# Performance work log

Measured on AMD Instinct MI355X. Metric: run time of the kernel, lower is better.

The kernel has to match this reference:

```python
import jax, jax.numpy as jnp
import numpy as np

N0, N1, N2, D, FANOUT = 900000, 43008, 2048, 64, 20


def setup_inputs() -> dict:
    key = jax.random.key(0)
    ks = jax.random.split(key, 8)
    x = jax.random.normal(ks[0], (N0, D), jnp.float32)
    edge_src0 = jax.random.randint(ks[1], (N1 * FANOUT,), 0, N0, jnp.int32)
    edge_dst0 = jax.random.randint(ks[2], (N1 * FANOUT,), 0, N1, jnp.int32)
    edge_src1 = jax.random.randint(ks[3], (N2 * FANOUT,), 0, N1, jnp.int32)
    edge_dst1 = jax.random.randint(ks[4], (N2 * FANOUT,), 0, N2, jnp.int32)
    # torch Linear(2D, D): store transposed as [2D, D] for x @ w + b
    w0 = jax.random.normal(ks[5], (2 * D, D), jnp.float32) * 0.05
    w1 = jax.random.normal(ks[6], (2 * D, D), jnp.float32) * 0.05
    b0 = jnp.zeros((D,), jnp.float32)
    b1 = jnp.zeros((D,), jnp.float32)
    return {"x": x, "w0": w0, "b0": b0, "w1": w1, "b1": b1,
            "edge_src0": edge_src0, "edge_dst0": edge_dst0,
            "edge_src1": edge_src1, "edge_dst1": edge_dst1,
            "n1": N1, "n2": N2}


def _sage_layer(h, src, dst, n_tgt, w, b, relu):
    # gather neighbor features [E, D]
    source_x = h[src]
    # scatter-mean into targets (torch_scatter reduce='mean' with zero init:
    # targets with no incoming edges stay 0)
    summ = jax.ops.segment_sum(source_x, dst, num_segments=n_tgt)
    cnt = jax.ops.segment_sum(jnp.ones((src.shape[0], 1), h.dtype), dst,
                              num_segments=n_tgt)
    aggr = summ / jnp.maximum(cnt, 1.0)
    out = jnp.concatenate([h[:n_tgt], aggr], axis=1) @ w + b
    return jax.nn.relu(out) if relu else out


def reference(x, w0, b0, w1, b1, edge_src0, edge_dst0, edge_src1, edge_dst1, n1, n2):
    # dropout is identity in eval mode
    h = _sage_layer(x, edge_src0, edge_dst0, n1, w0, b0, relu=True)
    out = _sage_layer(h, edge_src1, edge_dst1, n2, w1, b1, relu=False)
    return out
```

## Files before the change

kernel.cpp:

```cpp
#include <hip/hip_runtime.h>


#define D 64
constexpr int N1c = 43008;
constexpr int N2c = 2048;
constexpr int CAP = 64;

static __device__ __forceinline__ float readlane_f(float v, int l) {
    return __builtin_bit_cast(float, __builtin_amdgcn_readlane(__builtin_bit_cast(int, v), l));
}

__global__ void fill2_kernel(const int* __restrict__ es0, const int* __restrict__ ed0, int E0,
                             const int* __restrict__ es1, const int* __restrict__ ed1, int E1,
                             int* __restrict__ deg0, int* __restrict__ bucket0,
                             int* __restrict__ deg1, int* __restrict__ bucket1) {
    int t = blockIdx.x * blockDim.x + threadIdx.x;
    if (t < E0) {
        int d = ed0[t];
        int pos = atomicAdd(&deg0[d], 1);
        if (pos < CAP) bucket0[(size_t)d * CAP + pos] = es0[t];
    } else if (t - E0 < E1) {
        int e = t - E0;
        int d = ed1[e];
        int pos = atomicAdd(&deg1[d], 1);
        if (pos < CAP) bucket1[(size_t)d * CAP + pos] = es1[e];
    }
}

template <int BASE>
static __device__ __forceinline__ float slots32(int dg, int sidx,
                                                const float* __restrict__ feat,
                                                int lane) {
    float a0 = 0.f, a1 = 0.f, a2 = 0.f, a3 = 0.f;
#pragma unroll
    for (int j = 0; j < 32; j += 4) {
        int s0 = __builtin_amdgcn_readlane(sidx, BASE + j + 0);
        int s1 = __builtin_amdgcn_readlane(sidx, BASE + j + 1);
        int s2 = __builtin_amdgcn_readlane(sidx, BASE + j + 2);
        int s3 = __builtin_amdgcn_readlane(sidx, BASE + j + 3);
        float v0 = feat[(size_t)s0 * D + lane];
        float v1 = feat[(size_t)s1 * D + lane];
        float v2 = feat[(size_t)s2 * D + lane];
        float v3 = feat[(size_t)s3 * D + lane];
        a0 += (BASE + j + 0 < dg) ? v0 : 0.f;
        a1 += (BASE + j + 1 < dg) ? v1 : 0.f;
        a2 += (BASE + j + 2 < dg) ? v2 : 0.f;
        a3 += (BASE + j + 3 < dg) ? v3 : 0.f;
    }
    return (a0 + a1) + (a2 + a3);
}

__global__ void __launch_bounds__(256)
aggr_kernel(const float* __restrict__ feat,
            const int* __restrict__ deg, const int* __restrict__ bucket,
            float* __restrict__ aggr, int nrows) {
    int i = blockIdx.x * 4 + (threadIdx.x >> 6);
    int lane = threadIdx.x & 63;
    if (i >= nrows) return;
    int dgt = deg[i];
    int dg = dgt > CAP ? CAP : dgt;

    int sidx = (lane < dg) ? bucket[(size_t)i * CAP + lane] : 0;

    float sum = slots32<0>(dg, sidx, feat, lane);
    if (dg > 32)
        sum += slots32<32>(dg, sidx, feat, lane);

    float inv = 1.0f / fmaxf((float)dgt, 1.0f);
    aggr[(size_t)i * D + lane] = sum * inv;
}

__global__ void __launch_bounds__(256)
dense_kernel(const float* __restrict__ self_feat, const float* __restrict__ aggr,
             const float* __restrict__ w, const float* __restrict__ b,
             float* __restrict__ out, int nrows, int do_relu) {
    __shared__ float wlds[2 * D * D];
    int tid = threadIdx.x;
    {
        const float4* wsrc = (const float4*)w;
        float4* wdst = (float4*)wlds;
#pragma unroll
        for (int t = 0; t < 8; ++t)
            wdst[t * 256 + tid] = wsrc[t * 256 + tid];
    }
    __syncthreads();

    int wv = tid >> 6, lane = tid & 63;
    int i0 = (blockIdx.x * 4 + wv) * 4;
    if (i0 >= nrows) return;

    float x0 = self_feat[(size_t)(i0 + 0) * D + lane];
    float x1 = self_feat[(size_t)(i0 + 1) * D + lane];
    float x2 = self_feat[(size_t)(i0 + 2) * D + lane];
    float x3 = self_feat[(size_t)(i0 + 3) * D + lane];
    float g0 = aggr[(size_t)(i0 + 0) * D + lane];
    float g1 = aggr[(size_t)(i0 + 1) * D + lane];
    float g2 = aggr[(size_t)(i0 + 2) * D + lane];
    float g3 = aggr[(size_t)(i0 + 3) * D + lane];

    float bb = b[lane];
    float o0 = bb, o1 = bb, o2 = bb, o3 = bb;

#pragma unroll 16
    for (int k = 0; k < D; ++k) {
        float ws = wlds[k * D + lane];
        float wa = wlds[(D + k) * D + lane];
        o0 += readlane_f(x0, k) * ws + readlane_f(g0, k) * wa;
        o1 += readlane_f(x1, k) * ws + readlane_f(g1, k) * wa;
        o2 += readlane_f(x2, k) * ws + readlane_f(g2, k) * wa;
        o3 += readlane_f(x3, k) * ws + readlane_f(g3, k) * wa;
    }
    if (do_relu) {
        o0 = fmaxf(o0, 0.f); o1 = fmaxf(o1, 0.f);
        o2 = fmaxf(o2, 0.f); o3 = fmaxf(o3, 0.f);
    }
    out[(size_t)(i0 + 0) * D + lane] = o0;
    out[(size_t)(i0 + 1) * D + lane] = o1;
    out[(size_t)(i0 + 2) * D + lane] = o2;
    out[(size_t)(i0 + 3) * D + lane] = o3;
}

extern "C" void kernel_launch(void* const* d_in, const int* in_sizes, int n_in,
                              void* d_out, int out_size, void* d_ws, size_t ws_size,
                              hipStream_t stream) {
    const float* x   = (const float*)d_in[0];
    const float* w0  = (const float*)d_in[1];
    const float* b0  = (const float*)d_in[2];
    const float* w1  = (const float*)d_in[3];
    const float* b1  = (const float*)d_in[4];
    const int* es0   = (const int*)d_in[5];
    const int* ed0   = (const int*)d_in[6];
    const int* es1   = (const int*)d_in[7];
    const int* ed1   = (const int*)d_in[8];
    const int E0 = in_sizes[5];
    const int E1 = in_sizes[7];

    int* deg0    = (int*)d_ws;
    int* deg1    = deg0 + N1c;
    int* bucket0 = deg1 + N2c;
    int* bucket1 = bucket0 + (size_t)N1c * CAP;
    float* ag0   = (float*)(bucket1 + (size_t)N2c * CAP);
    float* h     = ag0 + (size_t)N1c * D;
    float* ag1   = h + (size_t)N1c * D;

    hipMemsetAsync(d_ws, 0, (size_t)(N1c + N2c) * sizeof(int), stream);

    int total = E0 + E1;
    fill2_kernel<<<(total + 255) / 256, 256, 0, stream>>>(es0, ed0, E0, es1, ed1, E1,
                                                          deg0, bucket0, deg1, bucket1);

    aggr_kernel<<<N1c / 4, 256, 0, stream>>>(x, deg0, bucket0, ag0, N1c);
    dense_kernel<<<N1c / 16, 256, 0, stream>>>(x, ag0, w0, b0, h, N1c, 1);

    aggr_kernel<<<N2c / 4, 256, 0, stream>>>(h, deg1, bucket1, ag1, N2c);
    dense_kernel<<<N2c / 16, 256, 0, stream>>>(h, ag1, w1, b1, (float*)d_out, N2c, 0);
}
```

Measured before the change: 411.7 us.

## Fuse neighbor aggregation into dense layer kernel and vectorize edge bucketing

Merges the aggregation and dense-projection kernels into one per-layer kernel, so the aggregated features stay in registers and no intermediate buffer is written to or read back from global memory. The aggregation now always issues 32 or 64 gathers without per-slot masking. Invalid slots read row 0, and the extra contribution is subtracted afterwards, which can cause small floating-point differences. The bucketing kernel now processes four edges per thread with int4 loads, which assumes E0 and E1 are multiples of four and that the arrays are suitably aligned.

```diff
diff --git a/kernel.cpp b/kernel.cpp
--- a/kernel.cpp
+++ b/kernel.cpp
@@ -15,22 +15,33 @@
                              int* __restrict__ deg0, int* __restrict__ bucket0,
                              int* __restrict__ deg1, int* __restrict__ bucket1) {
     int t = blockIdx.x * blockDim.x + threadIdx.x;
-    if (t < E0) {
-        int d = ed0[t];
-        int pos = atomicAdd(&deg0[d], 1);
-        if (pos < CAP) bucket0[(size_t)d * CAP + pos] = es0[t];
-    } else if (t - E0 < E1) {
-        int e = t - E0;
-        int d = ed1[e];
-        int pos = atomicAdd(&deg1[d], 1);
-        if (pos < CAP) bucket1[(size_t)d * CAP + pos] = es1[e];
+    int base = t * 4;
+    if (base < E0) {
+        int4 d4 = *(const int4*)(ed0 + base);
+        int4 s4 = *(const int4*)(es0 + base);
+        int p;
+        p = atomicAdd(&deg0[d4.x], 1); if (p < CAP) bucket0[(size_t)d4.x * CAP + p] = s4.x;
+        p = atomicAdd(&deg0[d4.y], 1); if (p < CAP) bucket0[(size_t)d4.y * CAP + p] = s4.y;
+        p = atomicAdd(&deg0[d4.z], 1); if (p < CAP) bucket0[(size_t)d4.z * CAP + p] = s4.z;
+        p = atomicAdd(&deg0[d4.w], 1); if (p < CAP) bucket0[(size_t)d4.w * CAP + p] = s4.w;
+    } else {
+        int b1 = base - E0;
+        if (b1 < E1) {
+            int4 d4 = *(const int4*)(ed1 + b1);
+            int4 s4 = *(const int4*)(es1 + b1);
+            int p;
+            p = atomicAdd(&deg1[d4.x], 1); if (p < CAP) bucket1[(size_t)d4.x * CAP + p] = s4.x;
+            p = atomicAdd(&deg1[d4.y], 1); if (p < CAP) bucket1[(size_t)d4.y * CAP + p] = s4.y;
+            p = atomicAdd(&deg1[d4.z], 1); if (p < CAP) bucket1[(size_t)d4.z * CAP + p] = s4.z;
+            p = atomicAdd(&deg1[d4.w], 1); if (p < CAP) bucket1[(size_t)d4.w * CAP + p] = s4.w;
+        }
     }
 }
 
 template <int BASE>
-static __device__ __forceinline__ float slots32(int dg, int sidx,
-                                                const float* __restrict__ feat,
-                                                int lane) {
+static __device__ __forceinline__ float slots32u(int sidx,
+                                                 const float* __restrict__ feat,
+                                                 int lane) {
     float a0 = 0.f, a1 = 0.f, a2 = 0.f, a3 = 0.f;
 #pragma unroll
     for (int j = 0; j < 32; j += 4) {
@@ -38,42 +49,19 @@
         int s1 = __builtin_amdgcn_readlane(sidx, BASE + j + 1);
         int s2 = __builtin_amdgcn_readlane(sidx, BASE + j + 2);
         int s3 = __builtin_amdgcn_readlane(sidx, BASE + j + 3);
-        float v0 = feat[(size_t)s0 * D + lane];
-        float v1 = feat[(size_t)s1 * D + lane];
-        float v2 = feat[(size_t)s2 * D + lane];
-        float v3 = feat[(size_t)s3 * D + lane];
-        a0 += (BASE + j + 0 < dg) ? v0 : 0.f;
-        a1 += (BASE + j + 1 < dg) ? v1 : 0.f;
-        a2 += (BASE + j + 2 < dg) ? v2 : 0.f;
-        a3 += (BASE + j + 3 < dg) ? v3 : 0.f;
+        a0 += feat[(size_t)s0 * D + lane];
+        a1 += feat[(size_t)s1 * D + lane];
+        a2 += feat[(size_t)s2 * D + lane];
+        a3 += feat[(size_t)s3 * D + lane];
     }
     return (a0 + a1) + (a2 + a3);
 }
 
 __global__ void __launch_bounds__(256)
-aggr_kernel(const float* __restrict__ feat,
-            const int* __restrict__ deg, const int* __restrict__ bucket,
-            float* __restrict__ aggr, int nrows) {
-    int i = blockIdx.x * 4 + (threadIdx.x >> 6);
-    int lane = threadIdx.x & 63;
-    if (i >= nrows) return;
-    int dgt = deg[i];
-    int dg = dgt > CAP ? CAP : dgt;
-
-    int sidx = (lane < dg) ? bucket[(size_t)i * CAP + lane] : 0;
-
-    float sum = slots32<0>(dg, sidx, feat, lane);
-    if (dg > 32)
-        sum += slots32<32>(dg, sidx, feat, lane);
-
-    float inv = 1.0f / fmaxf((float)dgt, 1.0f);
-    aggr[(size_t)i * D + lane] = sum * inv;
-}
-
-__global__ void __launch_bounds__(256)
-dense_kernel(const float* __restrict__ self_feat, const float* __restrict__ aggr,
-             const float* __restrict__ w, const float* __restrict__ b,
-             float* __restrict__ out, int nrows, int do_relu) {
+fused_layer_kernel(const float* __restrict__ feat,
+                   const int* __restrict__ deg, const int* __restrict__ bucket,
+                   const float* __restrict__ w, const float* __restrict__ b,
+                   float* __restrict__ out, int do_relu) {
     __shared__ float wlds[2 * D * D];
     int tid = threadIdx.x;
     {
@@ -87,28 +75,34 @@
 
     int wv = tid >> 6, lane = tid & 63;
     int i0 = (blockIdx.x * 4 + wv) * 4;
-    if (i0 >= nrows) return;
 
-    float x0 = self_feat[(size_t)(i0 + 0) * D + lane];
-    float x1 = self_feat[(size_t)(i0 + 1) * D + lane];
-    float x2 = self_feat[(size_t)(i0 + 2) * D + lane];
-    float x3 = self_feat[(size_t)(i0 + 3) * D + lane];
-    float g0 = aggr[(size_t)(i0 + 0) * D + lane];
-    float g1 = aggr[(size_t)(i0 + 1) * D + lane];
-    float g2 = aggr[(size_t)(i0 + 2) * D + lane];
-    float g3 = aggr[(size_t)(i0 + 3) * D + lane];
+    float x0f = feat[lane];
+
+    float g[4], sf[4];
+#pragma unroll
+    for (int r = 0; r < 4; ++r) {
+        int i = i0 + r;
+        int dgt = deg[i];
+        int dg  = dgt > CAP ? CAP : dgt;
+        int sidx = (lane < dg) ? bucket[(size_t)i * CAP + lane] : 0;
+        float sum = slots32u<0>(sidx, feat, lane);
+        int issued = 32;
+        if (dg > 32) { sum += slots32u<32>(sidx, feat, lane); issued = 64; }
+        sum -= (float)(issued - dg) * x0f;
+        g[r]  = sum / fmaxf((float)dgt, 1.0f);
+        sf[r] = feat[(size_t)i * D + lane];
+    }
 
     float bb = b[lane];
     float o0 = bb, o1 = bb, o2 = bb, o3 = bb;
-
 #pragma unroll 16
     for (int k = 0; k < D; ++k) {
         float ws = wlds[k * D + lane];
         float wa = wlds[(D + k) * D + lane];
-        o0 += readlane_f(x0, k) * ws + readlane_f(g0, k) * wa;
-        o1 += readlane_f(x1, k) * ws + readlane_f(g1, k) * wa;
-        o2 += readlane_f(x2, k) * ws + readlane_f(g2, k) * wa;
-        o3 += readlane_f(x3, k) * ws + readlane_f(g3, k) * wa;
+        o0 += readlane_f(sf[0], k) * ws + readlane_f(g[0], k) * wa;
+        o1 += readlane_f(sf[1], k) * ws + readlane_f(g[1], k) * wa;
+        o2 += readlane_f(sf[2], k) * ws + readlane_f(g[2], k) * wa;
+        o3 += readlane_f(sf[3], k) * ws + readlane_f(g[3], k) * wa;
     }
     if (do_relu) {
         o0 = fmaxf(o0, 0.f); o1 = fmaxf(o1, 0.f);
@@ -139,19 +133,15 @@
     int* deg1    = deg0 + N1c;
     int* bucket0 = deg1 + N2c;
     int* bucket1 = bucket0 + (size_t)N1c * CAP;
-    float* ag0   = (float*)(bucket1 + (size_t)N2c * CAP);
-    float* h     = ag0 + (size_t)N1c * D;
-    float* ag1   = h + (size_t)N1c * D;
+    float* h     = (float*)(bucket1 + (size_t)N2c * CAP);
 
     hipMemsetAsync(d_ws, 0, (size_t)(N1c + N2c) * sizeof(int), stream);
 
-    int total = E0 + E1;
-    fill2_kernel<<<(total + 255) / 256, 256, 0, stream>>>(es0, ed0, E0, es1, ed1, E1,
-                                                          deg0, bucket0, deg1, bucket1);
+    int total4 = (E0 + E1) / 4;
+    fill2_kernel<<<(total4 + 255) / 256, 256, 0, stream>>>(es0, ed0, E0, es1, ed1, E1,
+                                                           deg0, bucket0, deg1, bucket1);
 
-    aggr_kernel<<<N1c / 4, 256, 0, stream>>>(x, deg0, bucket0, ag0, N1c);
-    dense_kernel<<<N1c / 16, 256, 0, stream>>>(x, ag0, w0, b0, h, N1c, 1);
-
-    aggr_kernel<<<N2c / 4, 256, 0, stream>>>(h, deg1, bucket1, ag1, N2c);
-    dense_kernel<<<N2c / 16, 256, 0, stream>>>(h, ag1, w1, b1, (float*)d_out, N2c, 0);
+    fused_layer_kernel<<<N1c / 16, 256, 0, stream>>>(x, deg0, bucket0, w0, b0, h, 1);
+    fused_layer_kernel<<<N2c / 16, 256, 0, stream>>>(h, deg1, bucket1, w1, b1,
+                                                     (float*)d_out, 0);
 }
```

Result: faster. 400.7 us (-2.7%).
